# Optimization experiments

Hardware: AMD Instinct MI355X
Metric: run time of the kernel (lower is better)

## Reference

```python
import jax, jax.numpy as jnp
import numpy as np

N, E, C_IN, C_OUT = 50000, 800000, 64, 64
BN_EPS = 1e-5


def _batchnorm(h, gamma, beta):
    # Training-mode BatchNorm1d: batch statistics over dim 0, biased variance.
    mean = h.mean(axis=0)
    var = h.var(axis=0)  # ddof=0, matches PyTorch normalization stats
    return gamma * (h - mean) * jax.lax.rsqrt(var + BN_EPS) + beta


def setup_inputs() -> dict:
    key = jax.random.key(0)
    ks = jax.random.split(key, 6)
    x = jax.random.normal(ks[0], (N, C_IN), dtype=jnp.float32)
    edge_index = jax.random.randint(ks[1], (2, E), 0, N, dtype=jnp.int32)
    edge_weight = jax.random.uniform(ks[2], (E,), dtype=jnp.float32)
    s1 = 1.0 / np.sqrt(C_IN).astype(np.float32)
    s2 = 1.0 / np.sqrt(2 * C_IN).astype(np.float32)
    pool_W = jax.random.uniform(ks[3], (C_IN, C_IN), jnp.float32, -s1, s1)
    pool_b = jnp.zeros((C_IN,), jnp.float32)
    final_W = jax.random.uniform(ks[4], (2 * C_IN, C_OUT), jnp.float32, -s2, s2)
    final_b = jnp.zeros((C_OUT,), jnp.float32)
    return {
        "x": x,
        "edge_index": edge_index,
        "edge_weight": edge_weight,
        "pool_W": pool_W,
        "pool_b": pool_b,
        "bn_pool_gamma": jnp.ones((C_IN,), jnp.float32),
        "bn_pool_beta": jnp.zeros((C_IN,), jnp.float32),
        "final_W": final_W,
        "final_b": final_b,
        "bn_final_gamma": jnp.ones((C_OUT,), jnp.float32),
        "bn_final_beta": jnp.zeros((C_OUT,), jnp.float32),
        "coef": jnp.float32(0.5),
    }


def reference(x, edge_index, edge_weight, pool_W, pool_b, bn_pool_gamma,
              bn_pool_beta, final_W, final_b, bn_final_gamma, bn_final_beta,
              coef):
    src, dst = edge_index[0], edge_index[1]
    # gather src node features, scale by edge weight  -> [E, C_IN]
    edge_feat = x[src] * (1.0 + coef * edge_weight[:, None])
    pooled = edge_feat @ pool_W + pool_b              # [E, C_IN]
    pooled = jax.nn.relu(_batchnorm(pooled, bn_pool_gamma, bn_pool_beta))
    # scatter-max into destination nodes; empty segments -> 0 (pooled >= 0)
    agg = jax.ops.segment_max(pooled, dst, num_segments=x.shape[0])
    agg = jnp.maximum(agg, 0.0)                       # fill -inf (empty) with 0
    h = jnp.concatenate([x, agg], axis=-1) @ final_W + final_b  # [N, C_OUT]
    h = _batchnorm(h, bn_final_gamma, bn_final_beta)
    return jax.nn.relu(h)
```

## Files before the change

### kernel.cpp

```cpp
#include <hip/hip_runtime.h>
#include <hip/hip_fp16.h>
#include <math.h>
#include <float.h>

#define BN_EPS 1e-5f
#define SLOTS 64
#define SB 256


typedef __attribute__((ext_vector_type(8))) short bf16x8;
typedef __attribute__((ext_vector_type(4))) float f32x4;

__device__ inline unsigned short f2bf(float f) {
    unsigned u = __float_as_uint(f);
    return (unsigned short)((u + 0x7fffu + ((u >> 16) & 1u)) >> 16);
}
__device__ inline float bf2f(unsigned short h) {
    return __uint_as_float(((unsigned)h) << 16);
}

__global__ __launch_bounds__(256, 4) void k_scatter_gemm(
        const int* __restrict__ src, const int* __restrict__ dst,
        const float* __restrict__ w, const float* __restrict__ coef_p,
        int* __restrict__ cnt, unsigned* __restrict__ csr, int E,
        const float* __restrict__ x, const float* __restrict__ W,
        unsigned short* __restrict__ ybf, int nrows, int gemmGrid) {
    __shared__ unsigned short Wt[64 * 72];
    if (blockIdx.x < SB) {
        const float coef = *coef_p;
        const int tid = blockIdx.x * 256 + threadIdx.x;
        const int stride4 = SB * 256 * 4;
        for (int base = tid * 4; base < E; base += stride4) {
            if (base + 3 < E) {
                int4   s4 = *(const int4*)(src + base);
                int4   d4 = *(const int4*)(dst + base);
                float4 w4 = *(const float4*)(w + base);
                int sn[4] = {s4.x, s4.y, s4.z, s4.w};
                int dn[4] = {d4.x, d4.y, d4.z, d4.w};
                float wv[4] = {w4.x, w4.y, w4.z, w4.w};
                unsigned hs[4];
                int pos[4];
#pragma unroll
                for (int j = 0; j < 4; ++j) {
                    float s = fmaf(coef, wv[j], 1.0f);
                    hs[j] = (unsigned)__half_as_ushort(__float2half(s));
                    pos[j] = atomicAdd(&cnt[dn[j]], 1);
                }
#pragma unroll
                for (int j = 0; j < 4; ++j)
                    if (pos[j] < SLOTS)
                        csr[(size_t)dn[j] * SLOTS + pos[j]] =
                            ((unsigned)sn[j] << 16) | hs[j];
            } else {
                for (int i = base; i < E; ++i) {
                    int sn = src[i], tn = dst[i];
                    float s = fmaf(coef, w[i], 1.0f);
                    unsigned hs = (unsigned)__half_as_ushort(__float2half(s));
                    int pos = atomicAdd(&cnt[tn], 1);
                    if (pos < SLOTS)
                        csr[(size_t)tn * SLOTS + pos] = ((unsigned)sn << 16) | hs;
                }
            }
        }
        return;
    }
    const int bid = blockIdx.x - SB;
    for (int i = threadIdx.x; i < 64 * 64; i += 256) {
        int k = i >> 6, n = i & 63;
        Wt[n * 72 + k] = f2bf(W[i]);
    }
    __syncthreads();
    const int lane = threadIdx.x & 63;
    const int wave = threadIdx.x >> 6;
    const int quad = lane >> 4;
    const int ln = lane & 15;
    bf16x8 Bf[2][4];
#pragma unroll
    for (int kc = 0; kc < 2; ++kc)
#pragma unroll
        for (int ct = 0; ct < 4; ++ct)
            Bf[kc][ct] = *(const bf16x8*)&Wt[(ct * 16 + ln) * 72 + kc * 32 + quad * 8];
    const int T = (nrows + 15) >> 4;
    const int gw = bid * 4 + wave;
    const int nw = gemmGrid * 4;
    for (int t = gw; t < T; t += nw) {
        const int row = t * 16 + ln;
        bf16x8 af[2];
        if (row < nrows) {
            const float* xr = x + (size_t)row * 64;
#pragma unroll
            for (int kc = 0; kc < 2; ++kc) {
                float4 p = *(const float4*)(xr + kc * 32 + quad * 8);
                float4 q = *(const float4*)(xr + kc * 32 + quad * 8 + 4);
                bf16x8 a;
                a[0] = (short)f2bf(p.x); a[1] = (short)f2bf(p.y);
                a[2] = (short)f2bf(p.z); a[3] = (short)f2bf(p.w);
                a[4] = (short)f2bf(q.x); a[5] = (short)f2bf(q.y);
                a[6] = (short)f2bf(q.z); a[7] = (short)f2bf(q.w);
                af[kc] = a;
            }
        } else {
            bf16x8 z;
#pragma unroll
            for (int j = 0; j < 8; ++j) z[j] = 0;
            af[0] = z; af[1] = z;
        }
        f32x4 acc[4];
#pragma unroll
        for (int ct = 0; ct < 4; ++ct) { acc[ct][0]=0.f; acc[ct][1]=0.f; acc[ct][2]=0.f; acc[ct][3]=0.f; }
#pragma unroll
        for (int ct = 0; ct < 4; ++ct) {
            acc[ct] = __builtin_amdgcn_mfma_f32_16x16x32_bf16(af[0], Bf[0][ct], acc[ct], 0, 0, 0);
            acc[ct] = __builtin_amdgcn_mfma_f32_16x16x32_bf16(af[1], Bf[1][ct], acc[ct], 0, 0, 0);
        }
#pragma unroll
        for (int r = 0; r < 4; ++r) {
            int ro = t * 16 + quad * 4 + r;
            if (ro < nrows) {
#pragma unroll
                for (int ct = 0; ct < 4; ++ct)
                    ybf[(size_t)ro * 64 + ct * 16 + ln] = f2bf(acc[ct][r]);
            }
        }
    }
}

__global__ __launch_bounds__(256) void k_gather_max(const unsigned short* __restrict__ ybf,
                             const unsigned* __restrict__ csr, const int* __restrict__ cnt,
                             float* __restrict__ M, float* __restrict__ partials, int nrows) {
    int t = blockIdx.x * blockDim.x + threadIdx.x;
    int node = t >> 3;
    int sub = threadIdx.x & 7;
    int rg = threadIdx.x >> 3;
    int c0 = sub * 8;
    size_t base = (size_t)node * SLOTS;
    int dg = 0;
    if (node < nrows) { dg = cnt[node]; if (dg > SLOTS) dg = SLOTS; }
    float m[8], s1[8], s2[8];
#pragma unroll
    for (int c = 0; c < 8; ++c) { m[c] = -FLT_MAX; s1[c] = 0.0f; s2[c] = 0.0f; }
    for (int k0 = 0; k0 < dg; k0 += 8) {
        int kk = k0 + sub;
        unsigned pk = (kk < dg) ? csr[base + kk] : 0u;
        int rem = dg - k0;
        bf16x8 uv[8];
        float sv[8];
#pragma unroll
        for (int j = 0; j < 8; ++j) {
            unsigned r = (unsigned)__shfl((int)pk, j, 8);
            sv[j] = __half2float(__ushort_as_half((unsigned short)(r & 0xffffu)));
            uv[j] = *(const bf16x8*)&ybf[(size_t)(r >> 16) * 64 + c0];
        }
#pragma unroll
        for (int j = 0; j < 8; ++j) {
            if (j < rem) {
#pragma unroll
                for (int c = 0; c < 8; ++c) {
                    float v = sv[j] * bf2f((unsigned short)uv[j][c]);
                    m[c] = fmaxf(m[c], v);
                    s1[c] += v;
                    s2[c] = fmaf(v, v, s2[c]);
                }
            }
        }
    }
    if (node < nrows) {
        float4 a = make_float4(m[0], m[1], m[2], m[3]);
        float4 b = make_float4(m[4], m[5], m[6], m[7]);
        *(float4*)&M[(size_t)node * 64 + c0] = a;
        *(float4*)&M[(size_t)node * 64 + c0 + 4] = b;
    }
    __shared__ float red[32][72];
#pragma unroll
    for (int j = 0; j < 8; ++j) red[rg][c0 + j] = s1[j];
    __syncthreads();
    if (threadIdx.x < 64) {
        int c = threadIdx.x;
        float tt = 0.0f;
        for (int r = 0; r < 32; ++r) tt += red[r][c];
        partials[(size_t)blockIdx.x * 128 + c] = tt;
    }
    __syncthreads();
#pragma unroll
    for (int j = 0; j < 8; ++j) red[rg][c0 + j] = s2[j];
    __syncthreads();
    if (threadIdx.x < 64) {
        int c = threadIdx.x;
        float tt = 0.0f;
        for (int r = 0; r < 32; ++r) tt += red[r][c];
        partials[(size_t)blockIdx.x * 128 + 64 + c] = tt;
    }
}

__global__ __launch_bounds__(256) void k_red1(const float* __restrict__ partials, int P,
                                              float* __restrict__ p2) {
    int c = threadIdx.x & 127;
    int half = threadIdx.x >> 7;
    float acc = 0.0f;
    for (int r = blockIdx.x * 2 + half; r < P; r += 256)
        acc += partials[(size_t)r * 128 + c];
    __shared__ float sh[256];
    sh[threadIdx.x] = acc;
    __syncthreads();
    if (half == 0) p2[(size_t)blockIdx.x * 128 + c] = sh[c] + sh[128 + c];
}

__global__ __launch_bounds__(1024) void k_red2(const float* __restrict__ p2,
                             const float* __restrict__ pool_b, const float* __restrict__ gamma,
                             const float* __restrict__ beta, float invE,
                             float* __restrict__ coef) {
    int c = threadIdx.x & 127;
    int seg = threadIdx.x >> 7;
    float acc = 0.0f;
    for (int r = seg; r < 128; r += 8) acc += p2[(size_t)r * 128 + c];
    __shared__ float red[8][128];
    red[seg][c] = acc;
    __syncthreads();
    if (seg == 0) {
        float tt = 0.0f;
#pragma unroll
        for (int s = 0; s < 8; ++s) tt += red[s][c];
        red[0][c] = tt;
    }
    __syncthreads();
    if (threadIdx.x < 64) {
        int c0 = threadIdx.x;
        float S1 = red[0][c0], S2 = red[0][64 + c0];
        float s1 = S1 * invE;
        float b = pool_b[c0];
        float mean = s1 + b;
        float ex2 = S2 * invE + 2.0f * b * s1 + b * b;
        float var = ex2 - mean * mean;
        float a = gamma[c0] * rsqrtf(var + BN_EPS);
        coef[c0] = a;
        coef[64 + c0] = beta[c0] - a * s1;
    }
}

__global__ __launch_bounds__(1024) void k_red2f(const float* __restrict__ p2,
                             const float* __restrict__ gamma, const float* __restrict__ beta,
                             float invN, float* __restrict__ coef) {
    int c = threadIdx.x & 127;
    int seg = threadIdx.x >> 7;
    float acc = 0.0f;
    for (int r = seg; r < 128; r += 8) acc += p2[(size_t)r * 128 + c];
    __shared__ float red[8][128];
    red[seg][c] = acc;
    __syncthreads();
    if (seg == 0) {
        float tt = 0.0f;
#pragma unroll
        for (int s = 0; s < 8; ++s) tt += red[s][c];
        red[0][c] = tt;
    }
    __syncthreads();
    if (threadIdx.x < 64) {
        int c0 = threadIdx.x;
        float mean = red[0][c0] * invN;
        float var = red[0][64 + c0] * invN - mean * mean;
        float a = gamma[c0] * rsqrtf(var + BN_EPS);
        coef[c0] = a;
        coef[64 + c0] = beta[c0] - a * mean;
    }
}

__global__ __launch_bounds__(256, 2) void k_final_gemm(const float* __restrict__ x,
                             const float* __restrict__ M, const float* __restrict__ coef,
                             const float* __restrict__ W, const float* __restrict__ b,
                             float* __restrict__ h, float* __restrict__ partials, int nrows) {
    __shared__ unsigned short Wt[64 * 136];
    __shared__ float hp[128];
    for (int i = threadIdx.x; i < 128 * 64; i += 256) {
        int k = i >> 6, n = i & 63;
        Wt[n * 136 + k] = f2bf(W[i]);
    }
    if (threadIdx.x < 128) hp[threadIdx.x] = 0.0f;
    __syncthreads();
    const int lane = threadIdx.x & 63;
    const int wave = threadIdx.x >> 6;
    const int quad = lane >> 4;
    const int ln = lane & 15;
    bf16x8 Bf[4][4];
#pragma unroll
    for (int kc = 0; kc < 4; ++kc)
#pragma unroll
        for (int ct = 0; ct < 4; ++ct)
            Bf[kc][ct] = *(const bf16x8*)&Wt[(ct * 16 + ln) * 136 + kc * 32 + quad * 8];
    float bias[4];
#pragma unroll
    for (int ct = 0; ct < 4; ++ct) bias[ct] = b[ct * 16 + ln];
    float ca[2][8], cd[2][8];
#pragma unroll
    for (int g = 0; g < 2; ++g) {
        int ch = g * 32 + quad * 8;
#pragma unroll
        for (int j = 0; j < 8; ++j) {
            ca[g][j] = coef[ch + j];
            cd[g][j] = coef[64 + ch + j];
        }
    }
    float ls1[4] = {0, 0, 0, 0}, ls2[4] = {0, 0, 0, 0};
    const int T = (nrows + 15) >> 4;
    const int gw = blockIdx.x * 4 + wave;
    const int nw = gridDim.x * 4;
    for (int t = gw; t < T; t += nw) {
        const int row = t * 16 + ln;
        bf16x8 af[4];
        if (row < nrows) {
            const float* xr = x + (size_t)row * 64;
#pragma unroll
            for (int kc = 0; kc < 2; ++kc) {
                float4 p = *(const float4*)(xr + kc * 32 + quad * 8);
                float4 q = *(const float4*)(xr + kc * 32 + quad * 8 + 4);
                bf16x8 a;
                a[0] = (short)f2bf(p.x); a[1] = (short)f2bf(p.y);
                a[2] = (short)f2bf(p.z); a[3] = (short)f2bf(p.w);
                a[4] = (short)f2bf(q.x); a[5] = (short)f2bf(q.y);
                a[6] = (short)f2bf(q.z); a[7] = (short)f2bf(q.w);
                af[kc] = a;
            }
            const float* mr = M + (size_t)row * 64;
#pragma unroll
            for (int g = 0; g < 2; ++g) {
                const float* mp = mr + g * 32 + quad * 8;
                float4 p = *(const float4*)mp;
                float4 q = *(const float4*)(mp + 4);
                float v[8] = {p.x, p.y, p.z, p.w, q.x, q.y, q.z, q.w};
                bf16x8 a;
#pragma unroll
                for (int j = 0; j < 8; ++j)
                    a[j] = (short)f2bf(fmaxf(fmaf(ca[g][j], v[j], cd[g][j]), 0.0f));
                af[2 + g] = a;
            }
        } else {
            bf16x8 z;
#pragma unroll
            for (int j = 0; j < 8; ++j) z[j] = 0;
#pragma unroll
            for (int kc = 0; kc < 4; ++kc) af[kc] = z;
        }
        f32x4 acc[4];
#pragma unroll
        for (int ct = 0; ct < 4; ++ct) { acc[ct][0]=0.f; acc[ct][1]=0.f; acc[ct][2]=0.f; acc[ct][3]=0.f; }
#pragma unroll
        for (int kc = 0; kc < 4; ++kc)
#pragma unroll
            for (int ct = 0; ct < 4; ++ct)
                acc[ct] = __builtin_amdgcn_mfma_f32_16x16x32_bf16(af[kc], Bf[kc][ct], acc[ct], 0, 0, 0);
#pragma unroll
        for (int r = 0; r < 4; ++r) {
            int ro = t * 16 + quad * 4 + r;
            if (ro < nrows) {
#pragma unroll
                for (int ct = 0; ct < 4; ++ct) {
                    float hv = acc[ct][r] + bias[ct];
                    h[(size_t)ro * 64 + ct * 16 + ln] = hv;
                    ls1[ct] += hv;
                    ls2[ct] = fmaf(hv, hv, ls2[ct]);
                }
            }
        }
    }
#pragma unroll
    for (int ct = 0; ct < 4; ++ct) {
        atomicAdd(&hp[ct * 16 + ln], ls1[ct]);
        atomicAdd(&hp[64 + ct * 16 + ln], ls2[ct]);
    }
    __syncthreads();
    if (threadIdx.x < 128)
        partials[(size_t)blockIdx.x * 128 + threadIdx.x] = hp[threadIdx.x];
}

__global__ __launch_bounds__(256) void k_bn_out(const float* __restrict__ h,
                         const float* __restrict__ coef,
                         float* __restrict__ out, int nrows) {
    const int idx = blockIdx.x * blockDim.x + threadIdx.x;
    const int total = nrows * 16;
    if (idx >= total) return;
    const int c0 = (idx & 15) * 4;
    const float4 hv = *(const float4*)(h + (size_t)idx * 4);
    float4 o;
    float* op = (float*)&o;
    const float* hp = (const float*)&hv;
#pragma unroll
    for (int j = 0; j < 4; ++j) {
        const int c = c0 + j;
        op[j] = fmaxf(fmaf(coef[c], hp[j], coef[64 + c]), 0.0f);
    }
    *(float4*)(out + (size_t)idx * 4) = o;
}

extern "C" void kernel_launch(void* const* d_in, const int* in_sizes, int n_in,
                              void* d_out, int out_size, void* d_ws, size_t ws_size,
                              hipStream_t stream) {
    const float* x       = (const float*)d_in[0];
    const int*   eidx    = (const int*)d_in[1];
    const float* ew      = (const float*)d_in[2];
    const float* pool_W  = (const float*)d_in[3];
    const float* pool_b  = (const float*)d_in[4];
    const float* g1      = (const float*)d_in[5];
    const float* b1      = (const float*)d_in[6];
    const float* final_W = (const float*)d_in[7];
    const float* final_b = (const float*)d_in[8];
    const float* g2      = (const float*)d_in[9];
    const float* b2      = (const float*)d_in[10];
    const float* coef    = (const float*)d_in[11];

    const int N = in_sizes[0] / 64;
    const int E = in_sizes[1] / 2;
    const int* src = eidx;
    const int* dst = eidx + E;

    const int PG  = (N * 8 + 255) / 256;
    const int T   = (N + 15) / 16;
    const int nbT = (T + 3) / 4;

    unsigned* ws = (unsigned*)d_ws;
    int*   cnt      = (int*)ws;
    float* bncoef   = (float*)(ws + (size_t)N);
    float* coef2    = (float*)(ws + (size_t)N + 128);
    float* p2       = (float*)(ws + (size_t)N + 256);
    float* p2F      = p2 + 16384;
    float* partialsG= p2F + 16384;
    float* partialsF= partialsG + (size_t)PG * 128;
    unsigned short* ybf = (unsigned short*)(partialsF + (size_t)nbT * 128);
    unsigned* csrF  = (unsigned*)ybf + (size_t)32 * N;
    float* M        = (float*)(csrF + (size_t)SLOTS * N);

    hipMemsetAsync(cnt, 0, (size_t)N * 4, stream);

    k_scatter_gemm<<<SB + nbT, 256, 0, stream>>>(src, dst, ew, coef, cnt, csrF, E,
                                                 x, pool_W, ybf, N, nbT);
    k_gather_max<<<PG, 256, 0, stream>>>(ybf, csrF, cnt, M, partialsG, N);
    k_red1   <<<128, 256, 0, stream>>>(partialsG, PG, p2);
    k_red2   <<<1, 1024, 0, stream>>>(p2, pool_b, g1, b1, 1.0f / (float)E, bncoef);
    k_final_gemm<<<nbT, 256, 0, stream>>>(x, M, bncoef, final_W, final_b,
                                          (float*)d_out, partialsF, N);
    k_red1   <<<128, 256, 0, stream>>>(partialsF, nbT, p2F);
    k_red2f  <<<1, 1024, 0, stream>>>(p2F, g2, b2, 1.0f / (float)N, coef2);
    k_bn_out <<<(N * 16 + 255) / 256, 256, 0, stream>>>((const float*)d_out, coef2,
                                                        (float*)d_out, N);
}
```

Measured before the change: 200.9 us.

## Split final GEMM and precompute x@W_top in the scatter kernel

Splits the final GEMM along K: the x·W_top part (plus bias) is computed as extra blocks in the first scatter/pool-GEMM kernel, where it can overlap with the atomic scatter. The final GEMM then handles only the normalized aggregate half (K=64) and adds the precomputed fp32 partial read back from memory. This halves the MFMA work and the weight footprint of the final kernel, which now allows higher occupancy. The cost is an extra N×64 fp32 write and read.

```diff
diff --git a/kernel.cpp b/kernel.cpp
--- a/kernel.cpp
+++ b/kernel.cpp
@@ -23,8 +23,10 @@
         const int* __restrict__ src, const int* __restrict__ dst,
         const float* __restrict__ w, const float* __restrict__ coef_p,
         int* __restrict__ cnt, unsigned* __restrict__ csr, int E,
-        const float* __restrict__ x, const float* __restrict__ W,
-        unsigned short* __restrict__ ybf, int nrows, int gemmGrid) {
+        const float* __restrict__ x, const float* __restrict__ Wp,
+        unsigned short* __restrict__ ybf,
+        const float* __restrict__ Wf, const float* __restrict__ fb,
+        float* __restrict__ hx, int nrows, int g1) {
     __shared__ unsigned short Wt[64 * 72];
     if (blockIdx.x < SB) {
         const float coef = *coef_p;
@@ -64,10 +66,13 @@
         }
         return;
     }
-    const int bid = blockIdx.x - SB;
+    const int gb = blockIdx.x - SB;
+    const int hp_ = (gb >= g1) ? 1 : 0;
+    const int bid = hp_ ? gb - g1 : gb;
+    const float* Wsrc = hp_ ? Wf : Wp;
     for (int i = threadIdx.x; i < 64 * 64; i += 256) {
         int k = i >> 6, n = i & 63;
-        Wt[n * 72 + k] = f2bf(W[i]);
+        Wt[n * 72 + k] = f2bf(Wsrc[i]);
     }
     __syncthreads();
     const int lane = threadIdx.x & 63;
@@ -80,9 +85,12 @@
 #pragma unroll
         for (int ct = 0; ct < 4; ++ct)
             Bf[kc][ct] = *(const bf16x8*)&Wt[(ct * 16 + ln) * 72 + kc * 32 + quad * 8];
+    float bias[4];
+#pragma unroll
+    for (int ct = 0; ct < 4; ++ct) bias[ct] = hp_ ? fb[ct * 16 + ln] : 0.0f;
     const int T = (nrows + 15) >> 4;
     const int gw = bid * 4 + wave;
-    const int nw = gemmGrid * 4;
+    const int nw = g1 * 4;
     for (int t = gw; t < T; t += nw) {
         const int row = t * 16 + ln;
         bf16x8 af[2];
@@ -117,9 +125,15 @@
         for (int r = 0; r < 4; ++r) {
             int ro = t * 16 + quad * 4 + r;
             if (ro < nrows) {
-#pragma unroll
-                for (int ct = 0; ct < 4; ++ct)
-                    ybf[(size_t)ro * 64 + ct * 16 + ln] = f2bf(acc[ct][r]);
+                if (hp_) {
+#pragma unroll
+                    for (int ct = 0; ct < 4; ++ct)
+                        hx[(size_t)ro * 64 + ct * 16 + ln] = acc[ct][r] + bias[ct];
+                } else {
+#pragma unroll
+                    for (int ct = 0; ct < 4; ++ct)
+                        ybf[(size_t)ro * 64 + ct * 16 + ln] = f2bf(acc[ct][r]);
+                }
             }
         }
     }
@@ -264,15 +278,15 @@
     }
 }
 
-__global__ __launch_bounds__(256, 2) void k_final_gemm(const float* __restrict__ x,
+__global__ __launch_bounds__(256, 4) void k_final_gemm(const float* __restrict__ hx,
                              const float* __restrict__ M, const float* __restrict__ coef,
-                             const float* __restrict__ W, const float* __restrict__ b,
+                             const float* __restrict__ Wb,
                              float* __restrict__ h, float* __restrict__ partials, int nrows) {
-    __shared__ unsigned short Wt[64 * 136];
+    __shared__ unsigned short Wt[64 * 72];
     __shared__ float hp[128];
-    for (int i = threadIdx.x; i < 128 * 64; i += 256) {
+    for (int i = threadIdx.x; i < 64 * 64; i += 256) {
         int k = i >> 6, n = i & 63;
-        Wt[n * 136 + k] = f2bf(W[i]);
+        Wt[n * 72 + k] = f2bf(Wb[i]);
     }
     if (threadIdx.x < 128) hp[threadIdx.x] = 0.0f;
     __syncthreads();
@@ -280,15 +294,12 @@
     const int wave = threadIdx.x >> 6;
     const int quad = lane >> 4;
     const int ln = lane & 15;
-    bf16x8 Bf[4][4];
-#pragma unroll
-    for (int kc = 0; kc < 4; ++kc)
+    bf16x8 Bf[2][4];
+#pragma unroll
+    for (int kc = 0; kc < 2; ++kc)
 #pragma unroll
         for (int ct = 0; ct < 4; ++ct)
-            Bf[kc][ct] = *(const bf16x8*)&Wt[(ct * 16 + ln) * 136 + kc * 32 + quad * 8];
-    float bias[4];
-#pragma unroll
-    for (int ct = 0; ct < 4; ++ct) bias[ct] = b[ct * 16 + ln];
+            Bf[kc][ct] = *(const bf16x8*)&Wt[(ct * 16 + ln) * 72 + kc * 32 + quad * 8];
     float ca[2][8], cd[2][8];
 #pragma unroll
     for (int g = 0; g < 2; ++g) {
@@ -305,20 +316,8 @@
     const int nw = gridDim.x * 4;
     for (int t = gw; t < T; t += nw) {
         const int row = t * 16 + ln;
-        bf16x8 af[4];
+        bf16x8 af[2];
         if (row < nrows) {
-            const float* xr = x + (size_t)row * 64;
-#pragma unroll
-            for (int kc = 0; kc < 2; ++kc) {
-                float4 p = *(const float4*)(xr + kc * 32 + quad * 8);
-                float4 q = *(const float4*)(xr + kc * 32 + quad * 8 + 4);
-                bf16x8 a;
-                a[0] = (short)f2bf(p.x); a[1] = (short)f2bf(p.y);
-                a[2] = (short)f2bf(p.z); a[3] = (short)f2bf(p.w);
-                a[4] = (short)f2bf(q.x); a[5] = (short)f2bf(q.y);
-                a[6] = (short)f2bf(q.z); a[7] = (short)f2bf(q.w);
-                af[kc] = a;
-            }
             const float* mr = M + (size_t)row * 64;
 #pragma unroll
             for (int g = 0; g < 2; ++g) {
@@ -330,20 +329,19 @@
 #pragma unroll
                 for (int j = 0; j < 8; ++j)
                     a[j] = (short)f2bf(fmaxf(fmaf(ca[g][j], v[j], cd[g][j]), 0.0f));
-                af[2 + g] = a;
+                af[g] = a;
             }
         } else {
             bf16x8 z;
 #pragma unroll
             for (int j = 0; j < 8; ++j) z[j] = 0;
-#pragma unroll
-            for (int kc = 0; kc < 4; ++kc) af[kc] = z;
+            af[0] = z; af[1] = z;
         }
         f32x4 acc[4];
 #pragma unroll
         for (int ct = 0; ct < 4; ++ct) { acc[ct][0]=0.f; acc[ct][1]=0.f; acc[ct][2]=0.f; acc[ct][3]=0.f; }
 #pragma unroll
-        for (int kc = 0; kc < 4; ++kc)
+        for (int kc = 0; kc < 2; ++kc)
 #pragma unroll
             for (int ct = 0; ct < 4; ++ct)
                 acc[ct] = __builtin_amdgcn_mfma_f32_16x16x32_bf16(af[kc], Bf[kc][ct], acc[ct], 0, 0, 0);
@@ -353,7 +351,7 @@
             if (ro < nrows) {
 #pragma unroll
                 for (int ct = 0; ct < 4; ++ct) {
-                    float hv = acc[ct][r] + bias[ct];
+                    float hv = acc[ct][r] + hx[(size_t)ro * 64 + ct * 16 + ln];
                     h[(size_t)ro * 64 + ct * 16 + ln] = hv;
                     ls1[ct] += hv;
                     ls2[ct] = fmaf(hv, hv, ls2[ct]);
@@ -426,15 +424,17 @@
     unsigned short* ybf = (unsigned short*)(partialsF + (size_t)nbT * 128);
     unsigned* csrF  = (unsigned*)ybf + (size_t)32 * N;
     float* M        = (float*)(csrF + (size_t)SLOTS * N);
+    float* hx       = M + (size_t)64 * N;
 
     hipMemsetAsync(cnt, 0, (size_t)N * 4, stream);
 
-    k_scatter_gemm<<<SB + nbT, 256, 0, stream>>>(src, dst, ew, coef, cnt, csrF, E,
-                                                 x, pool_W, ybf, N, nbT);
+    k_scatter_gemm<<<SB + 2 * nbT, 256, 0, stream>>>(src, dst, ew, coef, cnt, csrF, E,
+                                                     x, pool_W, ybf,
+                                                     final_W, final_b, hx, N, nbT);
     k_gather_max<<<PG, 256, 0, stream>>>(ybf, csrF, cnt, M, partialsG, N);
     k_red1   <<<128, 256, 0, stream>>>(partialsG, PG, p2);
     k_red2   <<<1, 1024, 0, stream>>>(p2, pool_b, g1, b1, 1.0f / (float)E, bncoef);
-    k_final_gemm<<<nbT, 256, 0, stream>>>(x, M, bncoef, final_W, final_b,
+    k_final_gemm<<<nbT, 256, 0, stream>>>(hx, M, bncoef, final_W + 64 * 64,
                                           (float*)d_out, partialsF, N);
     k_red1   <<<128, 256, 0, stream>>>(partialsF, nbT, p2F);
     k_red2f  <<<1, 1024, 0, stream>>>(p2F, g2, b2, 1.0f / (float)N, coef2);
```

After: 201.7 us. Within noise of the previous version (+0.4%).
